# Performance work log

Measured on AMD Instinct MI355X. Metric: run time of the kernel, lower is better.

## Reference

```python
import jax, jax.numpy as jnp
import numpy as np

NUM_HEAD = 16
MASKED_BIAS = -10000.0


def setup_inputs() -> dict:
    key = jax.random.key(0)
    k1, k2, k3 = jax.random.split(key, 3)
    B, M, N = 2, 2048, 1024
    x = jax.random.normal(k1, (B, M, N), dtype=jnp.float32)
    w_attn = jax.random.normal(k2, (N, 3 * N), dtype=jnp.float32) * 0.02
    w_proj = jax.random.normal(k3, (N, N), dtype=jnp.float32) * 0.02
    b_attn = jnp.zeros((3 * N,), dtype=jnp.float32)
    b_proj = jnp.zeros((N,), dtype=jnp.float32)
    return {"x": x, "w_attn": w_attn, "w_proj": w_proj,
            "b_attn": b_attn, "b_proj": b_proj}


def reference(x, w_attn, w_proj, b_attn, b_proj):
    B, M, N = x.shape
    H = NUM_HEAD
    d = N // H  # head dim
    # fused QKV projection: [B,M,3N]
    qkv = jnp.einsum('bmn,nd->bmd', x, w_attn) + b_attn
    q, k, v = jnp.split(qkv, 3, axis=-1)
    # split heads -> [B,H,M,d]
    q = q.reshape(B, M, H, d).transpose(0, 2, 1, 3)
    k = k.reshape(B, M, H, d).transpose(0, 2, 1, 3)
    v = v.reshape(B, M, H, d).transpose(0, 2, 1, 3)
    # scaled dot-product scores [B,H,M,M]
    scores = jnp.einsum('bhqd,bhkd->bhqk', q, k) / jnp.sqrt(jnp.float32(d))
    causal = jnp.tril(jnp.ones((M, M), dtype=bool))  # GPT-2 bias buffer
    scores = jnp.where(causal, scores, jnp.float32(MASKED_BIAS))
    attn = jax.nn.softmax(scores, axis=-1)
    # context [B,H,M,d] -> [B,M,N]
    ctx = jnp.einsum('bhqk,bhkd->bhqd', attn, v)
    ctx = ctx.transpose(0, 2, 1, 3).reshape(B, M, N)
    # output projection
    out = jnp.einsum('bmn,no->bmo', ctx, w_proj) + b_proj
    return out
```

## Files before the change

### kernel.cpp

```cpp
#include <hip/hip_runtime.h>

typedef __attribute__((ext_vector_type(8))) __bf16 bf16x8;
typedef __attribute__((ext_vector_type(4))) __bf16 bf16x4;
typedef __attribute__((ext_vector_type(4))) float f32x4;
typedef __attribute__((ext_vector_type(4))) short short4v;

__device__ __forceinline__ void async_copy16(const void* g, void* l) {
    __builtin_amdgcn_global_load_lds(
        (const __attribute__((address_space(1))) void*)g,
        (__attribute__((address_space(3))) void*)l, 16, 0, 0);
}

__global__ __launch_bounds__(256) void prep_k(
    const float* __restrict__ x, __bf16* __restrict__ xb,
    const float* __restrict__ wa, __bf16* __restrict__ wAt,
    const float* __restrict__ wp, __bf16* __restrict__ wPt)
{
    __shared__ float tile[32][33];
    const int bx = blockIdx.x;
    if (bx < 2048) {
        size_t i = ((size_t)bx * 256 + threadIdx.x) * 8;
        float4 a = *(const float4*)&x[i];
        float4 b = *(const float4*)&x[i + 4];
        bf16x8 o;
        o[0] = (__bf16)a.x; o[1] = (__bf16)a.y; o[2] = (__bf16)a.z; o[3] = (__bf16)a.w;
        o[4] = (__bf16)b.x; o[5] = (__bf16)b.y; o[6] = (__bf16)b.z; o[7] = (__bf16)b.w;
        *(bf16x8*)&xb[i] = o;
        return;
    }
    const float* src; __bf16* dst; int R, C, c0, r0;
    if (bx < 5120) {
        int id = bx - 2048;
        src = wa; dst = wAt; R = 1024; C = 3072;
        c0 = (id % 96) * 32; r0 = (id / 96) * 32;
    } else {
        int id = bx - 5120;
        src = wp; dst = wPt; R = 1024; C = 1024;
        c0 = (id & 31) * 32; r0 = (id >> 5) * 32;
    }
    int tx = threadIdx.x & 31, ty = threadIdx.x >> 5;
    for (int i = ty; i < 32; i += 8)
        tile[i][tx] = src[(size_t)(r0 + i) * C + (c0 + tx)];
    __syncthreads();
    for (int i = ty; i < 32; i += 8)
        dst[(size_t)(c0 + i) * R + (r0 + tx)] = (__bf16)tile[tx][i];
}

template <int MODE, int TN>
__global__ __launch_bounds__(256) void gemm_bt(
    const __bf16* __restrict__ A, const __bf16* __restrict__ Bt,
    const float* __restrict__ bias, int K,
    __bf16* __restrict__ O0, __bf16* __restrict__ O1, __bf16* __restrict__ O2,
    float* __restrict__ Of)
{
    constexpr int NJ = TN / 32;
    __shared__ __align__(16) __bf16 lds_a[128 * 32];
    __shared__ __align__(16) __bf16 lds_b[TN * 32];
    const int row0 = blockIdx.x * 128;
    const int col0 = blockIdx.y * TN;
    const int tid  = threadIdx.x;
    const int lane = tid & 63;
    const int w    = tid >> 6;
    const int wm   = (w >> 1) * 64, wn = (w & 1) * (TN / 2);
    const int quad = lane >> 4, l16 = lane & 15;

    f32x4 acc[4][NJ] = {};
    for (int kb = 0; kb < K; kb += 32) {
#pragma unroll
        for (int t = 0; t < 2; ++t) {
            int s = t * 256 + tid;
            int L = s >> 3, c = (s & 7) ^ (L & 7);
            int row = 2 * L + (c >> 2), ch = c & 3;
            async_copy16(&A[(size_t)(row0 + row) * K + kb + ch * 8],
                         (char*)lds_a + (t * 256 + w * 64) * 16);
        }
#pragma unroll
        for (int t = 0; t < TN / 64; ++t) {
            int s = t * 256 + tid;
            int L = s >> 3, c = (s & 7) ^ (L & 7);
            int row = 2 * L + (c >> 2), ch = c & 3;
            async_copy16(&Bt[(size_t)(col0 + row) * K + kb + ch * 8],
                         (char*)lds_b + (t * 256 + w * 64) * 16);
        }
        __syncthreads();
        bf16x8 af[4], bfr[NJ];
#pragma unroll
        for (int i = 0; i < 4; ++i) {
            int r = wm + i * 16 + l16;
            int L = r >> 1, g = ((r & 1) * 4 + quad) ^ (L & 7);
            af[i] = *(const bf16x8*)&lds_a[L * 64 + g * 8];
        }
#pragma unroll
        for (int j = 0; j < NJ; ++j) {
            int r = wn + j * 16 + l16;
            int L = r >> 1, g = ((r & 1) * 4 + quad) ^ (L & 7);
            bfr[j] = *(const bf16x8*)&lds_b[L * 64 + g * 8];
        }
#pragma unroll
        for (int i = 0; i < 4; ++i)
#pragma unroll
            for (int j = 0; j < NJ; ++j)
                acc[i][j] = __builtin_amdgcn_mfma_f32_16x16x32_bf16(
                    af[i], bfr[j], acc[i][j], 0, 0, 0);
        __syncthreads();
    }

#pragma unroll
    for (int i = 0; i < 4; ++i) {
        int grow = row0 + wm + i * 16 + quad * 4;
#pragma unroll
        for (int j = 0; j < NJ; ++j) {
            int gcol = col0 + wn + j * 16 + l16;
            float bv = bias[gcol];
            if constexpr (MODE == 0) {
                int which = gcol >> 10;
                int n  = gcol & 1023;
                int hh = n >> 6, dd = n & 63;
                int bb = grow >> 11, mm0 = grow & 2047;
                int bhh = bb * 16 + hh;
                if (which == 2) {
                    bf16x4 pk;
#pragma unroll
                    for (int r = 0; r < 4; ++r)
                        pk[r] = (__bf16)(acc[i][j][r] + bv);
                    *(bf16x4*)&O2[((size_t)bhh * 64 + dd) * 2048 + mm0] = pk;
                } else {
#pragma unroll
                    for (int r = 0; r < 4; ++r) {
                        float v = acc[i][j][r] + bv;
                        if (which == 0)
                            O0[((size_t)bhh * 2048 + mm0 + r) * 64 + dd] =
                                (__bf16)(v * 0.18033688011112042f);
                        else
                            O1[((size_t)bhh * 2048 + mm0 + r) * 64 + dd] =
                                (__bf16)v;
                    }
                }
            } else {
#pragma unroll
                for (int r = 0; r < 4; ++r) {
                    int gr = grow + r;
                    Of[(size_t)gr * 1024 + gcol] = acc[i][j][r] + bv;
                }
            }
        }
    }
}

__global__ __launch_bounds__(256) void attn_kernel(
    const __bf16* __restrict__ Qh, const __bf16* __restrict__ Kh,
    const __bf16* __restrict__ Vt, __bf16* __restrict__ ctx)
{
    const int M = 2048, D = 64;
    const int bh = blockIdx.x;
    const int qt = 31 - blockIdx.y;
    const int b = bh >> 4, h = bh & 15;
    const int tid = threadIdx.x, lane = tid & 63, w = tid >> 6;
    const int quad = lane >> 4, l16 = lane & 15;

    const int q0 = qt * 64;
    const int nIter = qt + 1;

    __shared__ __align__(16) __bf16 lds_k[2][64 * 64];
    __shared__ __align__(16) __bf16 lds_v[2][64 * 64];

    const __bf16* Qp = Qh + (size_t)bh * M * D;
    const __bf16* Kp = Kh + (size_t)bh * M * D;
    const __bf16* Vp = Vt + (size_t)bh * D * M;

    const int qw = q0 + w * 16;

    bf16x8 qf[2];
#pragma unroll
    for (int c = 0; c < 2; ++c)
        qf[c] = *(const bf16x8*)
            &Qp[(size_t)(qw + l16) * D + c * 32 + quad * 8];

    f32x4 acc2[4] = {};
    f32x4 acc_s = {};
    const short4v ones2 = {0x3F80, 0x3F80, 0x3F80, 0x3F80};

    auto stage = [&](int pb, int kb) {
#pragma unroll
        for (int t = 0; t < 2; ++t) {
            int c = w * 128 + t * 64 + lane;
            int row = c >> 3, ch = c & 7;
            int gch = ch ^ (row & 7);
            async_copy16(&Kp[(size_t)(kb + row) * 64 + gch * 8],
                         (char*)&lds_k[pb][0] + (w * 128 + t * 64) * 16);
            async_copy16(&Vp[(size_t)row * M + kb + gch * 8],
                         (char*)&lds_v[pb][0] + (w * 128 + t * 64) * 16);
        }
    };

    stage(0, 0);

    for (int it = 0; it < nIter; ++it) {
        const int kb = it << 6;
        __syncthreads();
        if (it + 1 < nIter) stage((it + 1) & 1, kb + 64);
        const __bf16* kt = &lds_k[it & 1][0];
        const __bf16* vt = &lds_v[it & 1][0];

        f32x4 s[4];
#pragma unroll
        for (int t = 0; t < 4; ++t) {
            f32x4 tt = {};
#pragma unroll
            for (int c = 0; c < 2; ++c) {
                int ch = ((c << 2) + quad) ^ (l16 & 7);
                bf16x8 kf = *(const bf16x8*)
                    &kt[(((t << 4) + l16) << 6) + (ch << 3)];
                tt = __builtin_amdgcn_mfma_f32_16x16x32_bf16(
                    kf, qf[c], tt, 0, 0, 0);
            }
            s[t] = tt;
        }
        if (kb + 63 > qw) {
#pragma unroll
            for (int t = 0; t < 4; ++t)
#pragma unroll
                for (int r = 0; r < 4; ++r)
                    if (kb + t * 16 + quad * 4 + r > qw + l16)
                        s[t][r] = -1e30f;
        }
        short4v pf[4];
#pragma unroll
        for (int t = 0; t < 4; ++t) {
            bf16x4 pk;
#pragma unroll
            for (int r = 0; r < 4; ++r)
                pk[r] = (__bf16)exp2f(s[t][r]);
            pf[t] = *(short4v*)&pk;
        }
#pragma unroll
        for (int f = 0; f < 4; ++f)
#pragma unroll
            for (int t = 0; t < 4; ++t) {
                int row = (f << 4) + l16;
                int g = ((t << 1) + (quad >> 1)) ^ (row & 7);
                bf16x4 vv = *(const bf16x4*)
                    &vt[(row << 6) + (g << 3) + ((quad & 1) << 2)];
                acc2[f] = __builtin_amdgcn_mfma_f32_16x16x16bf16_1k(
                    *(short4v*)&vv, pf[t], acc2[f], 0, 0, 0);
            }
#pragma unroll
        for (int t = 0; t < 4; ++t)
            acc_s = __builtin_amdgcn_mfma_f32_16x16x16bf16_1k(
                ones2, pf[t], acc_s, 0, 0, 0);
    }

    __syncthreads();
    __bf16* ldsT = &lds_k[0][0];
    const float l = acc_s[0];
#pragma unroll
    for (int f = 0; f < 4; ++f) {
        bf16x4 ov;
#pragma unroll
        for (int r = 0; r < 4; ++r)
            ov[r] = (__bf16)(acc2[f][r] / l);
        *(bf16x4*)&ldsT[(w * 16 + l16) * 72 + f * 16 + quad * 4] = ov;
    }
    __syncthreads();
    {
        int qq = tid >> 2;
        int dp = (tid & 3) * 16;
        const __bf16* src = &ldsT[qq * 72 + dp];
        __bf16* dst = &ctx[((size_t)(b * 2048 + q0 + qq)) * 1024 + h * 64 + dp];
        *(bf16x8*)&dst[0] = *(const bf16x8*)&src[0];
        *(bf16x8*)&dst[8] = *(const bf16x8*)&src[8];
    }
}

extern "C" void kernel_launch(void* const* d_in, const int* in_sizes, int n_in,
                              void* d_out, int out_size, void* d_ws, size_t ws_size,
                              hipStream_t stream) {
    const float* x      = (const float*)d_in[0];
    const float* w_attn = (const float*)d_in[1];
    const float* w_proj = (const float*)d_in[2];
    const float* b_attn = (const float*)d_in[3];
    const float* b_proj = (const float*)d_in[4];
    float* out = (float*)d_out;

    char* ws = (char*)d_ws;
    __bf16* xb  = (__bf16*)(ws);
    __bf16* ctx = (__bf16*)(ws);
    __bf16* wAt = (__bf16*)(ws + 8388608);
    __bf16* wPt = (__bf16*)(ws + 14680064);
    __bf16* Vt  = (__bf16*)(ws + 16777216);
    __bf16* Qh  = (__bf16*)d_out;
    __bf16* Kh  = (__bf16*)d_out + 4194304;

    prep_k<<<6144, 256, 0, stream>>>(x, xb, w_attn, wAt, w_proj, wPt);
    gemm_bt<0, 128><<<dim3(32, 24), 256, 0, stream>>>(xb, wAt, b_attn, 1024,
                                                      Qh, Kh, Vt, nullptr);
    attn_kernel<<<dim3(32, 32), 256, 0, stream>>>(Qh, Kh, Vt, ctx);
    gemm_bt<1, 64><<<dim3(32, 16), 256, 0, stream>>>(ctx, wPt, b_proj, 1024,
                                                     nullptr, nullptr, nullptr, out);
}
```

Measured before the change: 183.8 us.

## Use 128-row query tiles with 8 waves sharing K/V staging in attention

The attention kernel now handles 128 query rows per block with 512 threads (8 waves), not 64 rows with 4 waves. Each K/V tile staged into shared memory is therefore reused by twice as many waves, halving global K/V traffic and the number of async copies per query row. Each thread now issues a single 16-byte copy per stage for K and for V, and waves whose rows all lie before the current key block skip the compute. The cost is causal load imbalance inside a block, since the lower-half waves sit idle on the final iteration while still joining the barriers, and the grid now has half as many, larger blocks.

```diff
diff --git a/kernel.cpp b/kernel.cpp
--- a/kernel.cpp
+++ b/kernel.cpp
@@ -147,22 +147,21 @@
     }
 }
 
-__global__ __launch_bounds__(256) void attn_kernel(
+__global__ __launch_bounds__(512) void attn_kernel(
     const __bf16* __restrict__ Qh, const __bf16* __restrict__ Kh,
     const __bf16* __restrict__ Vt, __bf16* __restrict__ ctx)
 {
     const int M = 2048, D = 64;
     const int bh = blockIdx.x;
-    const int qt = 31 - blockIdx.y;
+    const int yt = 15 - blockIdx.y;
     const int b = bh >> 4, h = bh & 15;
     const int tid = threadIdx.x, lane = tid & 63, w = tid >> 6;
     const int quad = lane >> 4, l16 = lane & 15;
 
-    const int q0 = qt * 64;
-    const int nIter = qt + 1;
-
-    __shared__ __align__(16) __bf16 lds_k[2][64 * 64];
-    __shared__ __align__(16) __bf16 lds_v[2][64 * 64];
+    const int q0 = yt * 128;
+    const int nIter = 2 * yt + 2;
+
+    __shared__ __align__(16) __bf16 smem[16384];
 
     const __bf16* Qp = Qh + (size_t)bh * M * D;
     const __bf16* Kp = Kh + (size_t)bh * M * D;
@@ -180,17 +179,14 @@
     f32x4 acc_s = {};
     const short4v ones2 = {0x3F80, 0x3F80, 0x3F80, 0x3F80};
 
+    const int srow = tid >> 3, spos = tid & 7;
+    const int sgch = spos ^ (srow & 7);
+
     auto stage = [&](int pb, int kb) {
-#pragma unroll
-        for (int t = 0; t < 2; ++t) {
-            int c = w * 128 + t * 64 + lane;
-            int row = c >> 3, ch = c & 7;
-            int gch = ch ^ (row & 7);
-            async_copy16(&Kp[(size_t)(kb + row) * 64 + gch * 8],
-                         (char*)&lds_k[pb][0] + (w * 128 + t * 64) * 16);
-            async_copy16(&Vp[(size_t)row * M + kb + gch * 8],
-                         (char*)&lds_v[pb][0] + (w * 128 + t * 64) * 16);
-        }
+        async_copy16(&Kp[(size_t)(kb + srow) * 64 + sgch * 8],
+                     (char*)smem + pb * 16384 + tid * 16);
+        async_copy16(&Vp[(size_t)srow * M + kb + sgch * 8],
+                     (char*)smem + pb * 16384 + 8192 + tid * 16);
     };
 
     stage(0, 0);
@@ -199,59 +195,62 @@
         const int kb = it << 6;
         __syncthreads();
         if (it + 1 < nIter) stage((it + 1) & 1, kb + 64);
-        const __bf16* kt = &lds_k[it & 1][0];
-        const __bf16* vt = &lds_v[it & 1][0];
-
-        f32x4 s[4];
-#pragma unroll
-        for (int t = 0; t < 4; ++t) {
-            f32x4 tt = {};
-#pragma unroll
-            for (int c = 0; c < 2; ++c) {
-                int ch = ((c << 2) + quad) ^ (l16 & 7);
-                bf16x8 kf = *(const bf16x8*)
-                    &kt[(((t << 4) + l16) << 6) + (ch << 3)];
-                tt = __builtin_amdgcn_mfma_f32_16x16x32_bf16(
-                    kf, qf[c], tt, 0, 0, 0);
-            }
-            s[t] = tt;
-        }
-        if (kb + 63 > qw) {
+        if (kb <= qw + 15) {
+            const __bf16* kt = (const __bf16*)
+                ((const char*)smem + (it & 1) * 16384);
+            const __bf16* vt = kt + 4096;
+
+            f32x4 s[4];
+#pragma unroll
+            for (int t = 0; t < 4; ++t) {
+                f32x4 tt = {};
+#pragma unroll
+                for (int c = 0; c < 2; ++c) {
+                    int ch = ((c << 2) + quad) ^ (l16 & 7);
+                    bf16x8 kf = *(const bf16x8*)
+                        &kt[(((t << 4) + l16) << 6) + (ch << 3)];
+                    tt = __builtin_amdgcn_mfma_f32_16x16x32_bf16(
+                        kf, qf[c], tt, 0, 0, 0);
+                }
+                s[t] = tt;
+            }
+            if (kb + 63 > qw) {
+#pragma unroll
+                for (int t = 0; t < 4; ++t)
+#pragma unroll
+                    for (int r = 0; r < 4; ++r)
+                        if (kb + t * 16 + quad * 4 + r > qw + l16)
+                            s[t][r] = -1e30f;
+            }
+            short4v pf[4];
+#pragma unroll
+            for (int t = 0; t < 4; ++t) {
+                bf16x4 pk;
+#pragma unroll
+                for (int r = 0; r < 4; ++r)
+                    pk[r] = (__bf16)exp2f(s[t][r]);
+                pf[t] = *(short4v*)&pk;
+            }
+#pragma unroll
+            for (int f = 0; f < 4; ++f)
+#pragma unroll
+                for (int t = 0; t < 4; ++t) {
+                    int row = (f << 4) + l16;
+                    int g = ((t << 1) + (quad >> 1)) ^ (row & 7);
+                    bf16x4 vv = *(const bf16x4*)
+                        &vt[(row << 6) + (g << 3) + ((quad & 1) << 2)];
+                    acc2[f] = __builtin_amdgcn_mfma_f32_16x16x16bf16_1k(
+                        *(short4v*)&vv, pf[t], acc2[f], 0, 0, 0);
+                }
 #pragma unroll
             for (int t = 0; t < 4; ++t)
-#pragma unroll
-                for (int r = 0; r < 4; ++r)
-                    if (kb + t * 16 + quad * 4 + r > qw + l16)
-                        s[t][r] = -1e30f;
-        }
-        short4v pf[4];
-#pragma unroll
-        for (int t = 0; t < 4; ++t) {
-            bf16x4 pk;
-#pragma unroll
-            for (int r = 0; r < 4; ++r)
-                pk[r] = (__bf16)exp2f(s[t][r]);
-            pf[t] = *(short4v*)&pk;
-        }
-#pragma unroll
-        for (int f = 0; f < 4; ++f)
-#pragma unroll
-            for (int t = 0; t < 4; ++t) {
-                int row = (f << 4) + l16;
-                int g = ((t << 1) + (quad >> 1)) ^ (row & 7);
-                bf16x4 vv = *(const bf16x4*)
-                    &vt[(row << 6) + (g << 3) + ((quad & 1) << 2)];
-                acc2[f] = __builtin_amdgcn_mfma_f32_16x16x16bf16_1k(
-                    *(short4v*)&vv, pf[t], acc2[f], 0, 0, 0);
-            }
-#pragma unroll
-        for (int t = 0; t < 4; ++t)
-            acc_s = __builtin_amdgcn_mfma_f32_16x16x16bf16_1k(
-                ones2, pf[t], acc_s, 0, 0, 0);
+                acc_s = __builtin_amdgcn_mfma_f32_16x16x16bf16_1k(
+                    ones2, pf[t], acc_s, 0, 0, 0);
+        }
     }
 
     __syncthreads();
-    __bf16* ldsT = &lds_k[0][0];
+    __bf16* ldsT = smem;
     const float l = acc_s[0];
 #pragma unroll
     for (int f = 0; f < 4; ++f) {
@@ -294,7 +293,7 @@
     prep_k<<<6144, 256, 0, stream>>>(x, xb, w_attn, wAt, w_proj, wPt);
     gemm_bt<0, 128><<<dim3(32, 24), 256, 0, stream>>>(xb, wAt, b_attn, 1024,
                                                       Qh, Kh, Vt, nullptr);
-    attn_kernel<<<dim3(32, 32), 256, 0, stream>>>(Qh, Kh, Vt, ctx);
+    attn_kernel<<<dim3(32, 16), 512, 0, stream>>>(Qh, Kh, Vt, ctx);
     gemm_bt<1, 64><<<dim3(32, 16), 256, 0, stream>>>(ctx, wPt, b_proj, 1024,
                                                      nullptr, nullptr, nullptr, out);
 }
```

New measurement: 184.5 us. About the same (+0.4%).
